# Kernel tuning notes

Measured on AMD Instinct MI355X. Metric: run time of the kernel, lower is better.

## Reference

```python
import jax, jax.numpy as jnp
import numpy as np

DIM = 128  # feature dim, used for 1/sqrt(dim) scaling


def setup_inputs() -> dict:
    key = jax.random.key(0)
    kq, kk, kv, kpq, kpk = jax.random.split(key, 5)
    B, S, D = 16, 2048, DIM
    return {
        "Q": jax.random.normal(kq, (B, S, D), dtype=jnp.float32),
        "K": jax.random.normal(kk, (B, S, D), dtype=jnp.float32),
        "V": jax.random.normal(kv, (B, S, D), dtype=jnp.float32),
        "p_q": jax.random.uniform(kpq, (B, S, 1), dtype=jnp.float32),
        "p_k": jax.random.uniform(kpk, (B, S, 1), dtype=jnp.float32),
    }


def reference(Q, K, V, p_q, p_k):
    # A: [B, Sq, Sk] scaled dot-product scores
    scale = 1.0 / jnp.sqrt(jnp.asarray(DIM, dtype=Q.dtype))
    A = jnp.einsum("bqd,bkd->bqk", Q, K) * scale
    # multiplicative pre-gate: p_q [B,Sq,1] * p_k^T [B,1,Sk]
    A = A * p_q * jnp.swapaxes(p_k, -2, -1)
    W = jax.nn.softmax(A, axis=-1)
    return jnp.einsum("bqk,bkd->bqd", W, V)
```

## Files before the change

kernel.cpp:

```cpp
#include <hip/hip_runtime.h>
#include <hip/hip_fp16.h>


typedef _Float16 f16x8 __attribute__((ext_vector_type(8)));
typedef float f32x16 __attribute__((ext_vector_type(16)));
typedef unsigned int u32x4 __attribute__((ext_vector_type(4)));

#define S_LEN 2048
#define DD 128
#define TILE_BYTES 16384
#define NT 32
#define NTH 16
#define PART_ROWS 32768
#define PART_STRIDE 4194304

#define EXP2(x) __builtin_amdgcn_exp2f(x)

__device__ __forceinline__ unsigned int pk2(float a, float b) {
  __half2 h = __float22half2_rn(make_float2(a, b));
  return __builtin_bit_cast(unsigned int, h);
}

__device__ __forceinline__ void st8(void* dst, const float v[8]) {
  u32x4 u;
  u[0] = pk2(v[0], v[1]);
  u[1] = pk2(v[2], v[3]);
  u[2] = pk2(v[4], v[5]);
  u[3] = pk2(v[6], v[7]);
  *(u32x4*)dst = u;
}

__device__ __forceinline__ void gld16(const void* g, void* l) {
  __builtin_amdgcn_global_load_lds(
      (const __attribute__((address_space(1))) unsigned int*)g,
      (__attribute__((address_space(3))) unsigned int*)l, 16, 0, 0);
}

__global__ __launch_bounds__(256) void prep_q_k(const float* __restrict__ Q,
                                                const float* __restrict__ pq,
                                                char* __restrict__ qh) {
  size_t i = ((size_t)blockIdx.x * 256 + threadIdx.x) * 8;
  const float g = pq[i >> 7] * 0.12751743343158394f;
  float4 a = *(const float4*)(Q + i);
  float4 b = *(const float4*)(Q + i + 4);
  float v[8] = {a.x * g, a.y * g, a.z * g, a.w * g,
                b.x * g, b.y * g, b.z * g, b.w * g};
  st8(qh + i * 2, v);
}

__global__ __launch_bounds__(256) void prep_kv(
    const float* __restrict__ K, const float* __restrict__ V,
    const float* __restrict__ pk, char* __restrict__ kimg,
    char* __restrict__ vimg) {
  __shared__ float vt[64 * 132];
  const int t = threadIdx.x;
  const int bid = blockIdx.x;
  const int bq = bid & 15;
  const int kt = bid >> 4;
  const size_t rowbase = (size_t)bq * S_LEN + kt * 64;

#pragma unroll
  for (int cc = 0; cc < 8; ++cc) {
    const int f = cc * 256 + t;
    const int row = f >> 5;
    const int col = (f & 31) * 4;
    *(float4*)(vt + row * 132 + col) = *(const float4*)(V + (rowbase + row) * DD + col);
  }

  char* kdst = kimg + (size_t)(bq * NT + kt) * TILE_BYTES;
#pragma unroll
  for (int cc = 0; cc < 4; ++cc) {
    const int p0 = (cc * 256 + t) * 16;
    const int key = p0 >> 8;
    const int d0 = ((p0 & 255) ^ ((key & 7) << 4)) >> 1;
    const float g = pk[rowbase + key];
    const float* src = K + (rowbase + key) * DD + d0;
    float4 a = *(const float4*)(src);
    float4 b = *(const float4*)(src + 4);
    float v[8] = {a.x * g, a.y * g, a.z * g, a.w * g,
                  b.x * g, b.y * g, b.z * g, b.w * g};
    st8(kdst + p0, v);
  }

  __syncthreads();

  char* vdst = vimg + (size_t)(bq * NT + kt) * TILE_BYTES;
#pragma unroll
  for (int cc = 0; cc < 4; ++cc) {
    const int p0 = (cc * 256 + t) * 16;
    const int dcol = p0 >> 7;
    const int key0 = ((p0 & 127) ^ ((dcol & 7) << 4)) >> 1;
    float v[8];
#pragma unroll
    for (int j = 0; j < 8; ++j) v[j] = vt[(key0 + j) * 132 + dcol];
    st8(vdst + p0, v);
  }
}

__global__ __launch_bounds__(512, 2) void attn_main(const char* __restrict__ qh,
                                                    const char* __restrict__ kimg,
                                                    const char* __restrict__ vimg,
                                                    _Float16* __restrict__ part,
                                                    float2* __restrict__ mlws) {
  __shared__ float4 ldsraw[4096];
  char* lds = (char*)ldsraw;
  const int tid = threadIdx.x;
  const int qs = tid >> 6;
  const int lane = tid & 63;
  const int c = lane & 31;
  const int h = lane >> 5;
  const int swz = (c & 7) << 4;
  const int bid = blockIdx.x;
  const int bq = 2 * (bid & 7) + ((bid >> 3) & 1);
  const int qt = (bid >> 4) & 7;
  const int kh = bid >> 7;
  const int q0 = qt * 256 + qs * 32;

  f16x8 qf[8];
  const char* qrow = qh + (size_t)(bq * S_LEN + q0 + c) * (DD * 2);
#pragma unroll
  for (int kc = 0; kc < 8; ++kc) qf[kc] = *(const f16x8*)(qrow + kc * 32 + h * 16);

  f32x16 acc[4];
#pragma unroll
  for (int d = 0; d < 4; ++d) {
#pragma unroll
    for (int r = 0; r < 16; ++r) acc[d][r] = 0.f;
  }
  float m_run = -1.0e30f, l_run = 0.f;

  const char* kb = kimg + (size_t)(bq * NT + kh * NTH) * TILE_BYTES;
  const char* vb = vimg + (size_t)(bq * NT + kh * NTH) * TILE_BYTES;

#pragma unroll
  for (int j = 0; j < 2; ++j) {
    gld16(kb + j * 8192 + tid * 16, lds + j * 8192 + tid * 16);
    gld16(vb + j * 8192 + tid * 16, lds + TILE_BYTES + j * 8192 + tid * 16);
  }

  for (int kt = 0; kt < NTH; ++kt) {
    __syncthreads();
    const int cur = (kt & 1) << 15;
    if (kt + 1 < NTH) {
      const int nxt = ((kt + 1) & 1) << 15;
      const char* kn = kb + (size_t)(kt + 1) * TILE_BYTES;
      const char* vn = vb + (size_t)(kt + 1) * TILE_BYTES;
#pragma unroll
      for (int j = 0; j < 2; ++j) {
        gld16(kn + j * 8192 + tid * 16, lds + nxt + j * 8192 + tid * 16);
        gld16(vn + j * 8192 + tid * 16, lds + nxt + TILE_BYTES + j * 8192 + tid * 16);
      }
    }
    const char* kl = lds + cur;
    const char* vl = lds + cur + TILE_BYTES;

    f32x16 s0, s1;
#pragma unroll
    for (int r = 0; r < 16; ++r) { s0[r] = 0.f; s1[r] = 0.f; }
    __builtin_amdgcn_s_setprio(1);
#pragma unroll
    for (int kc = 0; kc < 8; ++kc) {
      f16x8 k0 = *(const f16x8*)(kl + c * 256 + ((kc * 32 + h * 16) ^ swz));
      f16x8 k1 = *(const f16x8*)(kl + (32 + c) * 256 + ((kc * 32 + h * 16) ^ swz));
      s0 = __builtin_amdgcn_mfma_f32_32x32x16_f16(k0, qf[kc], s0, 0, 0, 0);
      s1 = __builtin_amdgcn_mfma_f32_32x32x16_f16(k1, qf[kc], s1, 0, 0, 0);
    }
    __builtin_amdgcn_s_setprio(0);

    float m0 = fmaxf(fmaxf(s0[0], s0[1]), fmaxf(s0[2], s0[3]));
    float m1 = fmaxf(fmaxf(s0[4], s0[5]), fmaxf(s0[6], s0[7]));
    float m2 = fmaxf(fmaxf(s0[8], s0[9]), fmaxf(s0[10], s0[11]));
    float m3 = fmaxf(fmaxf(s0[12], s0[13]), fmaxf(s0[14], s0[15]));
    float m4 = fmaxf(fmaxf(s1[0], s1[1]), fmaxf(s1[2], s1[3]));
    float m5 = fmaxf(fmaxf(s1[4], s1[5]), fmaxf(s1[6], s1[7]));
    float m6 = fmaxf(fmaxf(s1[8], s1[9]), fmaxf(s1[10], s1[11]));
    float m7 = fmaxf(fmaxf(s1[12], s1[13]), fmaxf(s1[14], s1[15]));
    m0 = fmaxf(m0, m1); m2 = fmaxf(m2, m3); m4 = fmaxf(m4, m5); m6 = fmaxf(m6, m7);
    float cm = fmaxf(fmaxf(m0, m2), fmaxf(m4, m6));
    cm = fmaxf(cm, __shfl_xor(cm, 32));
    if (__any(cm > m_run + 11.0f)) {
      const float mn = fmaxf(m_run, cm);
      const float al = EXP2(m_run - mn);
      m_run = mn;
      l_run *= al;
#pragma unroll
      for (int d = 0; d < 4; ++d) {
#pragma unroll
        for (int r = 0; r < 16; ++r) acc[d][r] *= al;
      }
    }
    float ps0 = 0.f, ps1 = 0.f;
#pragma unroll
    for (int r = 0; r < 16; ++r) {
      s0[r] = EXP2(s0[r] - m_run); ps0 += s0[r];
      s1[r] = EXP2(s1[r] - m_run); ps1 += s1[r];
    }
    l_run += ps0 + ps1;

#pragma unroll
    for (int kc = 0; kc < 4; ++kc) {
      const f32x16 pn = (kc < 2) ? s0 : s1;
      const int A = (kc & 1) * 8;
      const int Bb = A + 4;
      unsigned pA0 = pk2(pn[A + 0], pn[A + 1]);
      unsigned pA1 = pk2(pn[A + 2], pn[A + 3]);
      unsigned pB0 = pk2(pn[Bb + 0], pn[Bb + 1]);
      unsigned pB1 = pk2(pn[Bb + 2], pn[Bb + 3]);
      unsigned own0 = h ? pB0 : pA0;
      unsigned own1 = h ? pB1 : pA1;
      unsigned snd0 = h ? pA0 : pB0;
      unsigned snd1 = h ? pA1 : pB1;
      unsigned rcv0 = __shfl_xor(snd0, 32);
      unsigned rcv1 = __shfl_xor(snd1, 32);
      u32x4 pw;
      pw[0] = h ? rcv0 : own0;
      pw[1] = h ? rcv1 : own1;
      pw[2] = h ? own0 : rcv0;
      pw[3] = h ? own1 : rcv1;
      f16x8 pf = __builtin_bit_cast(f16x8, pw);
      __builtin_amdgcn_s_setprio(1);
#pragma unroll
      for (int d = 0; d < 4; ++d) {
        f16x8 vf = *(const f16x8*)(vl + (d * 32 + c) * 128 + ((kc * 32 + h * 16) ^ swz));
        acc[d] = __builtin_amdgcn_mfma_f32_32x32x16_f16(vf, pf, acc[d], 0, 0, 0);
      }
      __builtin_amdgcn_s_setprio(0);
    }
  }

  l_run += __shfl_xor(l_run, 32);
  const float w = 1.0f / l_run;

  __syncthreads();
  char* T = lds;
#pragma unroll
  for (int d = 0; d < 4; ++d) {
#pragma unroll
    for (int rr = 0; rr < 4; ++rr) {
      unsigned lo = pk2(acc[d][rr * 4 + 0] * w, acc[d][rr * 4 + 1] * w);
      unsigned hi = pk2(acc[d][rr * 4 + 2] * w, acc[d][rr * 4 + 3] * w);
      const int byte = (qs * 32 + c) * 256 + ((d * 64 + rr * 16 + h * 8) ^ swz);
      uint2 u; u.x = lo; u.y = hi;
      *(uint2*)(T + byte) = u;
    }
  }
  if (h == 0)
    mlws[(size_t)kh * PART_ROWS + (size_t)bq * S_LEN + qt * 256 + qs * 32 + c] =
        make_float2(m_run, l_run);
  __syncthreads();

  _Float16* pdst = part + (size_t)kh * PART_STRIDE +
                   ((size_t)bq * S_LEN + qt * 256) * 128;
#pragma unroll
  for (int p = 0; p < 8; ++p) {
    const int idx = p * 512 + tid;
    const int q = idx >> 4;
    const int o16 = (idx & 15) * 16;
    u32x4 v = *(const u32x4*)(T + q * 256 + (o16 ^ ((q & 7) << 4)));
    *(u32x4*)(pdst + q * 128 + (idx & 15) * 8) = v;
  }
}

__global__ __launch_bounds__(256) void merge2(const _Float16* __restrict__ part,
                                              const float2* __restrict__ mlws,
                                              float* __restrict__ out) {
  const int t = blockIdx.x * 256 + threadIdx.x;
  const int d0 = (t & 15) * 8;
  const int r = t >> 4;
  const float2 a = mlws[r];
  const float2 b = mlws[PART_ROWS + r];
  const float M = fmaxf(a.x, b.x);
  const float wa = a.y * EXP2(a.x - M);
  const float wb = b.y * EXP2(b.x - M);
  const float inv = 1.f / (wa + wb);
  const float fa = wa * inv, fb = wb * inv;
  const f16x8 pa = *(const f16x8*)(part + (size_t)r * 128 + d0);
  const f16x8 pb = *(const f16x8*)(part + PART_STRIDE + (size_t)r * 128 + d0);
  float4 o0, o1;
  o0.x = fa * (float)pa[0] + fb * (float)pb[0];
  o0.y = fa * (float)pa[1] + fb * (float)pb[1];
  o0.z = fa * (float)pa[2] + fb * (float)pb[2];
  o0.w = fa * (float)pa[3] + fb * (float)pb[3];
  o1.x = fa * (float)pa[4] + fb * (float)pb[4];
  o1.y = fa * (float)pa[5] + fb * (float)pb[5];
  o1.z = fa * (float)pa[6] + fb * (float)pb[6];
  o1.w = fa * (float)pa[7] + fb * (float)pb[7];
  float* orow = out + (size_t)r * 128 + d0;
  *(float4*)orow = o0;
  *(float4*)(orow + 4) = o1;
}

extern "C" void kernel_launch(void* const* d_in, const int* in_sizes, int n_in,
                              void* d_out, int out_size, void* d_ws, size_t ws_size,
                              hipStream_t stream) {
  const float* Q = (const float*)d_in[0];
  const float* K = (const float*)d_in[1];
  const float* V = (const float*)d_in[2];
  const float* pq = (const float*)d_in[3];
  const float* pk = (const float*)d_in[4];
  float* out = (float*)d_out;
  char* ws = (char*)d_ws;
  char* qh = ws;
  char* kimg = ws + (8u << 20);
  char* vimg = ws + (16u << 20);
  _Float16* part = (_Float16*)(ws + (24u << 20));
  float2* mlws = (float2*)(ws + (42u << 20));

  prep_q_k<<<2048, 256, 0, stream>>>(Q, pq, qh);
  prep_kv<<<512, 256, 0, stream>>>(K, V, pk, kimg, vimg);
  attn_main<<<256, 512, 0, stream>>>(qh, kimg, vimg, part, mlws);
  merge2<<<2048, 256, 0, stream>>>(part, mlws, out);
}
```

Baseline: 67.87 us.

## Use 4-deep LDS ring, fragment-order K/V images, and staggered wave ping-pong

The preprocessing kernel now writes K and V tiles in MFMA fragment order, so the main kernel can read them from LDS with linear per-lane offsets instead of XOR-swizzled addresses. The main kernel's LDS grows to a 4-slot ring for K and V, prefetching two tiles ahead. Waves 4-7 are offset by one phase and run QK(t) after softmax/PV(t-1), so the two halves of the block alternate between MFMA-heavy and exp-heavy work. The larger LDS footprint (128KB) may block two workgroups per CU despite launch_bounds(512,2). The linear fragment reads may also cause LDS bank conflicts.

```diff
diff --git a/kernel.cpp b/kernel.cpp
--- a/kernel.cpp
+++ b/kernel.cpp
@@ -13,6 +13,7 @@
 #define NTH 16
 #define PART_ROWS 32768
 #define PART_STRIDE 4194304
+#define LDS_VRING 65536
 
 #define EXP2(x) __builtin_amdgcn_exp2f(x)
 
@@ -70,16 +71,20 @@
   char* kdst = kimg + (size_t)(bq * NT + kt) * TILE_BYTES;
 #pragma unroll
   for (int cc = 0; cc < 4; ++cc) {
-    const int p0 = (cc * 256 + t) * 16;
-    const int key = p0 >> 8;
-    const int d0 = ((p0 & 255) ^ ((key & 7) << 4)) >> 1;
+    const int i = cc * 256 + t;
+    const int cI = i & 31;
+    const int ksub = (i >> 5) & 1;
+    const int hI = (i >> 6) & 1;
+    const int kcI = i >> 7;
+    const int key = ksub * 32 + cI;
+    const int d0 = kcI * 16 + hI * 8;
     const float g = pk[rowbase + key];
     const float* src = K + (rowbase + key) * DD + d0;
     float4 a = *(const float4*)(src);
     float4 b = *(const float4*)(src + 4);
     float v[8] = {a.x * g, a.y * g, a.z * g, a.w * g,
                   b.x * g, b.y * g, b.z * g, b.w * g};
-    st8(kdst + p0, v);
+    st8(kdst + i * 16, v);
   }
 
   __syncthreads();
@@ -87,13 +92,17 @@
   char* vdst = vimg + (size_t)(bq * NT + kt) * TILE_BYTES;
 #pragma unroll
   for (int cc = 0; cc < 4; ++cc) {
-    const int p0 = (cc * 256 + t) * 16;
-    const int dcol = p0 >> 7;
-    const int key0 = ((p0 & 127) ^ ((dcol & 7) << 4)) >> 1;
+    const int i = cc * 256 + t;
+    const int cI = i & 31;
+    const int dI = (i >> 5) & 3;
+    const int hI = (i >> 7) & 1;
+    const int kcI = i >> 8;
+    const int key0 = kcI * 16 + hI * 8;
+    const int dcol = dI * 32 + cI;
     float v[8];
 #pragma unroll
-    for (int j = 0; j < 8; ++j) v[j] = vt[(key0 + j) * 132 + dcol];
-    st8(vdst + p0, v);
+    for (int e = 0; e < 8; ++e) v[e] = vt[(key0 + e) * 132 + dcol];
+    st8(vdst + i * 16, v);
   }
 }
 
@@ -102,10 +111,10 @@
                                                     const char* __restrict__ vimg,
                                                     _Float16* __restrict__ part,
                                                     float2* __restrict__ mlws) {
-  __shared__ float4 ldsraw[4096];
+  __shared__ float4 ldsraw[8192];
   char* lds = (char*)ldsraw;
   const int tid = threadIdx.x;
-  const int qs = tid >> 6;
+  const int wid = tid >> 6;
   const int lane = tid & 63;
   const int c = lane & 31;
   const int h = lane >> 5;
@@ -114,7 +123,7 @@
   const int bq = 2 * (bid & 7) + ((bid >> 3) & 1);
   const int qt = (bid >> 4) & 7;
   const int kh = bid >> 7;
-  const int q0 = qt * 256 + qs * 32;
+  const int q0 = qt * 256 + wid * 32;
 
   f16x8 qf[8];
   const char* qrow = qh + (size_t)(bq * S_LEN + q0 + c) * (DD * 2);
@@ -128,45 +137,38 @@
     for (int r = 0; r < 16; ++r) acc[d][r] = 0.f;
   }
   float m_run = -1.0e30f, l_run = 0.f;
+  f32x16 s0, s1;
 
   const char* kb = kimg + (size_t)(bq * NT + kh * NTH) * TILE_BYTES;
   const char* vb = vimg + (size_t)(bq * NT + kh * NTH) * TILE_BYTES;
 
-#pragma unroll
-  for (int j = 0; j < 2; ++j) {
-    gld16(kb + j * 8192 + tid * 16, lds + j * 8192 + tid * 16);
-    gld16(vb + j * 8192 + tid * 16, lds + TILE_BYTES + j * 8192 + tid * 16);
-  }
-
-  for (int kt = 0; kt < NTH; ++kt) {
-    __syncthreads();
-    const int cur = (kt & 1) << 15;
-    if (kt + 1 < NTH) {
-      const int nxt = ((kt + 1) & 1) << 15;
-      const char* kn = kb + (size_t)(kt + 1) * TILE_BYTES;
-      const char* vn = vb + (size_t)(kt + 1) * TILE_BYTES;
-#pragma unroll
-      for (int j = 0; j < 2; ++j) {
-        gld16(kn + j * 8192 + tid * 16, lds + nxt + j * 8192 + tid * 16);
-        gld16(vn + j * 8192 + tid * 16, lds + nxt + TILE_BYTES + j * 8192 + tid * 16);
-      }
-    }
-    const char* kl = lds + cur;
-    const char* vl = lds + cur + TILE_BYTES;
-
-    f32x16 s0, s1;
+  auto STAGE = [&](int t) {
+    const char* kn = kb + (size_t)t * TILE_BYTES;
+    const char* vn = vb + (size_t)t * TILE_BYTES;
+    char* kd = lds + (t & 3) * TILE_BYTES;
+    char* vd = lds + LDS_VRING + (t & 3) * TILE_BYTES;
+    gld16(kn + tid * 16, kd + tid * 16);
+    gld16(kn + 8192 + tid * 16, kd + 8192 + tid * 16);
+    gld16(vn + tid * 16, vd + tid * 16);
+    gld16(vn + 8192 + tid * 16, vd + 8192 + tid * 16);
+  };
+
+  auto QK = [&](int t) {
+    const char* kA = lds + (t & 3) * TILE_BYTES + h * 1024 + c * 16;
 #pragma unroll
     for (int r = 0; r < 16; ++r) { s0[r] = 0.f; s1[r] = 0.f; }
     __builtin_amdgcn_s_setprio(1);
 #pragma unroll
     for (int kc = 0; kc < 8; ++kc) {
-      f16x8 k0 = *(const f16x8*)(kl + c * 256 + ((kc * 32 + h * 16) ^ swz));
-      f16x8 k1 = *(const f16x8*)(kl + (32 + c) * 256 + ((kc * 32 + h * 16) ^ swz));
+      f16x8 k0 = *(const f16x8*)(kA + kc * 2048);
+      f16x8 k1 = *(const f16x8*)(kA + kc * 2048 + 512);
       s0 = __builtin_amdgcn_mfma_f32_32x32x16_f16(k0, qf[kc], s0, 0, 0, 0);
       s1 = __builtin_amdgcn_mfma_f32_32x32x16_f16(k1, qf[kc], s1, 0, 0, 0);
     }
     __builtin_amdgcn_s_setprio(0);
-
+  };
+
+  auto SMPV = [&](int t) {
     float m0 = fmaxf(fmaxf(s0[0], s0[1]), fmaxf(s0[2], s0[3]));
     float m1 = fmaxf(fmaxf(s0[4], s0[5]), fmaxf(s0[6], s0[7]));
     float m2 = fmaxf(fmaxf(s0[8], s0[9]), fmaxf(s0[10], s0[11]));
@@ -197,6 +199,7 @@
     }
     l_run += ps0 + ps1;
 
+    const char* vA = lds + LDS_VRING + (t & 3) * TILE_BYTES + h * 2048 + c * 16;
 #pragma unroll
     for (int kc = 0; kc < 4; ++kc) {
       const f32x16 pn = (kc < 2) ? s0 : s1;
@@ -221,17 +224,41 @@
       __builtin_amdgcn_s_setprio(1);
 #pragma unroll
       for (int d = 0; d < 4; ++d) {
-        f16x8 vf = *(const f16x8*)(vl + (d * 32 + c) * 128 + ((kc * 32 + h * 16) ^ swz));
+        f16x8 vf = *(const f16x8*)(vA + kc * 4096 + d * 512);
         acc[d] = __builtin_amdgcn_mfma_f32_32x32x16_f16(vf, pf, acc[d], 0, 0, 0);
       }
       __builtin_amdgcn_s_setprio(0);
     }
-  }
+  };
+
+  STAGE(0);
+  STAGE(1);
+  __syncthreads();
+
+  if (wid < 4) {
+    for (int t = 0; t < NTH; ++t) {
+      if (t + 2 < NTH) STAGE(t + 2);
+      QK(t);
+      SMPV(t);
+      __syncthreads();
+    }
+  } else {
+    STAGE(2);
+    QK(0);
+    __syncthreads();
+    for (int t = 1; t < NTH; ++t) {
+      if (t + 2 < NTH) STAGE(t + 2);
+      SMPV(t - 1);
+      QK(t);
+      __syncthreads();
+    }
+    SMPV(NTH - 1);
+  }
+  __syncthreads();
 
   l_run += __shfl_xor(l_run, 32);
   const float w = 1.0f / l_run;
 
-  __syncthreads();
   char* T = lds;
 #pragma unroll
   for (int d = 0; d < 4; ++d) {
@@ -239,13 +266,13 @@
     for (int rr = 0; rr < 4; ++rr) {
       unsigned lo = pk2(acc[d][rr * 4 + 0] * w, acc[d][rr * 4 + 1] * w);
       unsigned hi = pk2(acc[d][rr * 4 + 2] * w, acc[d][rr * 4 + 3] * w);
-      const int byte = (qs * 32 + c) * 256 + ((d * 64 + rr * 16 + h * 8) ^ swz);
+      const int byte = (wid * 32 + c) * 256 + ((d * 64 + rr * 16 + h * 8) ^ swz);
       uint2 u; u.x = lo; u.y = hi;
       *(uint2*)(T + byte) = u;
     }
   }
   if (h == 0)
-    mlws[(size_t)kh * PART_ROWS + (size_t)bq * S_LEN + qt * 256 + qs * 32 + c] =
+    mlws[(size_t)kh * PART_ROWS + (size_t)bq * S_LEN + qt * 256 + wid * 32 + c] =
         make_float2(m_run, l_run);
   __syncthreads();
 
```

Result: no change. 68.64 us (+1.1%).
